# Optimization experiments

Measured on AMD Instinct MI355X. Metric: run time of the kernel, lower is better.

The kernel has to match this reference:

```python
import jax, jax.numpy as jnp
import numpy as np

K = 32
TEMPERATURE = 0.1
RTOL, ATOL = 1e-5, 1e-5


def _embed(x, W1, b1, W2, b2, W3, b3):
    h = jax.nn.gelu(x @ W1.T + b1, approximate=False)
    h = jax.nn.gelu(h @ W2.T + b2, approximate=False)
    return jax.nn.sigmoid(h @ W3.T + b3)


def setup_inputs() -> dict:
    key = jax.random.key(0)
    ks = jax.random.split(key, 9)
    Q, N, D_IN, D_E = 256, 16384, 256, 64
    s = lambda fan_in: 1.0 / np.sqrt(fan_in)
    return {
        "x": jax.random.normal(ks[0], (Q, D_IN), jnp.float32),
        "support_x": jax.random.normal(ks[1], (N, D_IN), jnp.float32),
        "support_labels": jax.random.uniform(ks[2], (N, 1), jnp.float32),
        "W1": jax.random.normal(ks[3], (D_E, D_IN), jnp.float32) * s(D_IN),
        "b1": jax.random.normal(ks[4], (D_E,), jnp.float32) * s(D_IN),
        "W2": jax.random.normal(ks[5], (D_E, D_E), jnp.float32) * s(D_E),
        "b2": jax.random.normal(ks[6], (D_E,), jnp.float32) * s(D_E),
        "W3": jax.random.normal(ks[7], (D_E, D_E), jnp.float32) * s(D_E),
        "b3": jax.random.normal(ks[8], (D_E,), jnp.float32) * s(D_E),
    }


def reference(x, support_x, support_labels, W1, b1, W2, b2, W3, b3):
    # query embeddings [Q, D]; support embeddings [N, D] (set_support is no_grad)
    q = _embed(x, W1, b1, W2, b2, W3, b3)
    s = jax.lax.stop_gradient(_embed(support_x, W1, b1, W2, b2, W3, b3))
    # torch.cdist p=2 via expanded squared distances
    d2 = (jnp.sum(q * q, -1)[:, None] + jnp.sum(s * s, -1)[None, :]
          - 2.0 * (q @ s.T))
    dist = jnp.sqrt(jnp.maximum(d2, 0.0))  # [Q, N]
    # isclose mask: |q - s| <= atol + rtol*|s|, all over feature dim
    close = jnp.abs(q[:, None, :] - s[None, :, :]) <= (ATOL + RTOL * jnp.abs(s)[None, :, :])
    mask = jnp.all(close, axis=-1)  # [Q, N]
    dist = jnp.where(mask, jnp.inf, dist)
    # top-k smallest distances
    neg_top, idx = jax.lax.top_k(-dist, K)  # [Q, K]
    topd = -neg_top
    neighbor_labels = support_labels[idx].squeeze(-1)  # [Q, K]
    weights = jax.nn.softmax(-topd / TEMPERATURE, axis=1)
    return jnp.sum(weights * neighbor_labels, axis=1)  # [Q]
```

## Files before the change

kernel.cpp:

```cpp
#include <hip/hip_runtime.h>
#include <math.h>

#define D_IN   256
#define D_E    64
#define N_SUP  16384
#define NQ     256
#define KSEL   32
#define RTOLC  1e-5f
#define ATOLC  1e-5f
#define INV_T  10.0f

#define CHUNK  1024
#define NCH    16
#define QG     8
#define NQG    32
#define EROWS  16

typedef unsigned long long ull;

__device__ __forceinline__ float gelu_exact(float x) {
    return 0.5f * x * (1.0f + erff(x * 0.70710678118654752440f));
}

__global__ __launch_bounds__(256, 4) void embed_kernel(
    const float* __restrict__ sx, const float* __restrict__ x,
    const float* __restrict__ W1, const float* __restrict__ b1,
    const float* __restrict__ W2, const float* __restrict__ b2,
    const float* __restrict__ W3, const float* __restrict__ b3,
    float* __restrict__ s_emb, float* __restrict__ s_norm,
    float* __restrict__ q_emb, float* __restrict__ q_norm)
{
    __shared__ float xc[2][64][17];
    __shared__ float wc[2][64][68];
    __shared__ float hA[64][17];
    __shared__ float nsq[16][17];

    const int tid = threadIdx.x;
    const int r   = tid & 15;
    const int fg4 = (tid >> 4) * 4;
    const bool isq = blockIdx.x >= (N_SUP / EROWS);
    const float* src = isq ? (x + (size_t)(blockIdx.x - N_SUP / EROWS) * EROWS * D_IN)
                           : (sx + (size_t)blockIdx.x * EROWS * D_IN);

    #define STAGE_X(kc_, b_)                                                   \
        {                                                                      \
            int row_ = tid >> 4, c4_ = tid & 15;                               \
            float4 v_ = *reinterpret_cast<const float4*>(                      \
                src + (size_t)row_ * D_IN + (kc_) * 64 + c4_ * 4);             \
            xc[b_][c4_ * 4 + 0][row_] = v_.x;                                  \
            xc[b_][c4_ * 4 + 1][row_] = v_.y;                                  \
            xc[b_][c4_ * 4 + 2][row_] = v_.z;                                  \
            xc[b_][c4_ * 4 + 3][row_] = v_.w;                                  \
        }
    #define STAGE_W1(kc_, b_)                                                  \
        {                                                                      \
            _Pragma("unroll")                                                  \
            for (int i_ = 0; i_ < 4; ++i_) {                                   \
                int g_ = i_ * 256 + tid;                                       \
                int f_ = g_ >> 4, c4_ = g_ & 15;                               \
                float4 w_ = *reinterpret_cast<const float4*>(                  \
                    W1 + (size_t)f_ * D_IN + (kc_) * 64 + c4_ * 4);            \
                wc[b_][c4_ * 4 + 0][f_] = w_.x;                                \
                wc[b_][c4_ * 4 + 1][f_] = w_.y;                                \
                wc[b_][c4_ * 4 + 2][f_] = w_.z;                                \
                wc[b_][c4_ * 4 + 3][f_] = w_.w;                                \
            }                                                                  \
        }

    STAGE_X(0, 0);
    STAGE_W1(0, 0);
    __syncthreads();

    float4 bv1 = *reinterpret_cast<const float4*>(b1 + fg4);
    float acc[4] = {bv1.x, bv1.y, bv1.z, bv1.w};
    for (int kc = 0; kc < 4; ++kc) {
        const int b = kc & 1;
        if (kc < 3) { STAGE_X(kc + 1, b ^ 1); STAGE_W1(kc + 1, b ^ 1); }
        #pragma unroll 8
        for (int k = 0; k < 64; ++k) {
            float xk = xc[b][k][r];
            float4 wv = *reinterpret_cast<const float4*>(&wc[b][k][fg4]);
            acc[0] = fmaf(wv.x, xk, acc[0]);
            acc[1] = fmaf(wv.y, xk, acc[1]);
            acc[2] = fmaf(wv.z, xk, acc[2]);
            acc[3] = fmaf(wv.w, xk, acc[3]);
        }
        __syncthreads();
    }
    #pragma unroll
    for (int i = 0; i < 4; ++i) hA[fg4 + i][r] = gelu_exact(acc[i]);
    #pragma unroll
    for (int i = 0; i < 4; ++i) {
        int g = i * 256 + tid;
        int f = g >> 4, c4 = g & 15;
        float4 w2 = *reinterpret_cast<const float4*>(W2 + (size_t)f * D_E + c4 * 4);
        wc[0][c4 * 4 + 0][f] = w2.x; wc[0][c4 * 4 + 1][f] = w2.y;
        wc[0][c4 * 4 + 2][f] = w2.z; wc[0][c4 * 4 + 3][f] = w2.w;
        float4 w3 = *reinterpret_cast<const float4*>(W3 + (size_t)f * D_E + c4 * 4);
        wc[1][c4 * 4 + 0][f] = w3.x; wc[1][c4 * 4 + 1][f] = w3.y;
        wc[1][c4 * 4 + 2][f] = w3.z; wc[1][c4 * 4 + 3][f] = w3.w;
    }
    __syncthreads();

    float4 bv2 = *reinterpret_cast<const float4*>(b2 + fg4);
    float a2[4] = {bv2.x, bv2.y, bv2.z, bv2.w};
    #pragma unroll 8
    for (int k = 0; k < D_E; ++k) {
        float hk = hA[k][r];
        float4 wv = *reinterpret_cast<const float4*>(&wc[0][k][fg4]);
        a2[0] = fmaf(wv.x, hk, a2[0]);
        a2[1] = fmaf(wv.y, hk, a2[1]);
        a2[2] = fmaf(wv.z, hk, a2[2]);
        a2[3] = fmaf(wv.w, hk, a2[3]);
    }
    #pragma unroll
    for (int i = 0; i < 4; ++i) xc[0][fg4 + i][r] = gelu_exact(a2[i]);
    __syncthreads();

    float4 bv3 = *reinterpret_cast<const float4*>(b3 + fg4);
    float a3[4] = {bv3.x, bv3.y, bv3.z, bv3.w};
    #pragma unroll 8
    for (int k = 0; k < D_E; ++k) {
        float hk = xc[0][k][r];
        float4 wv = *reinterpret_cast<const float4*>(&wc[1][k][fg4]);
        a3[0] = fmaf(wv.x, hk, a3[0]);
        a3[1] = fmaf(wv.y, hk, a3[1]);
        a3[2] = fmaf(wv.z, hk, a3[2]);
        a3[3] = fmaf(wv.w, hk, a3[3]);
    }
    float e[4];
    float np = 0.0f;
    #pragma unroll
    for (int i = 0; i < 4; ++i) {
        e[i] = 1.0f / (1.0f + expf(-a3[i]));
        np = fmaf(e[i], e[i], np);
    }

    const int rowg = (isq ? (blockIdx.x - N_SUP / EROWS) * EROWS : blockIdx.x * EROWS) + r;
    float* E   = isq ? q_emb  : s_emb;
    float* Nrm = isq ? q_norm : s_norm;
    *reinterpret_cast<float4*>(E + (size_t)rowg * D_E + fg4) =
        make_float4(e[0], e[1], e[2], e[3]);

    nsq[r][fg4 >> 2] = np;
    __syncthreads();
    if (tid < EROWS) {
        float s = nsq[tid][0];
        #pragma unroll
        for (int g = 1; g < 16; ++g) s += nsq[tid][g];
        const int rg = (isq ? (blockIdx.x - N_SUP / EROWS) * EROWS : blockIdx.x * EROWS) + tid;
        Nrm[rg] = s;
    }
    #undef STAGE_X
    #undef STAGE_W1
}

__global__ __launch_bounds__(512, 2) void knn_phaseA(
    const float* __restrict__ s_emb, const float* __restrict__ s_norm,
    const float* __restrict__ q_emb, const float* __restrict__ q_norm,
    const float* __restrict__ labels, ull* __restrict__ cand)
{
    __shared__ float tile[2][64 * 68];
    __shared__ float d2l[QG][1032];
    __shared__ float qs[QG][68];
    __shared__ float qn_l[QG];
    __shared__ ull   win_l[QG][KSEL];

    const int tid  = threadIdx.x;
    const int lane = tid & 63;
    const int wid  = tid >> 6;
    const int qg   = blockIdx.x >> 4;
    const int sc   = blockIdx.x & 15;

    {
        int q = tid >> 6, c = tid & 63;
        qs[q][c] = q_emb[(size_t)(qg * QG + q) * D_E + c];
        if (tid < QG) qn_l[tid] = q_norm[qg * QG + tid];
        #pragma unroll
        for (int i = 0; i < 2; ++i) {
            int g = i * 512 + tid;
            int row = g >> 4, c4 = g & 15;
            float4 v = *reinterpret_cast<const float4*>(
                s_emb + (size_t)(sc * CHUNK + row) * D_E + c4 * 4);
            *reinterpret_cast<float4*>(&tile[0][row * 68 + c4 * 4]) = v;
        }
    }
    __syncthreads();

    const int ql   = lane >> 3;
    const int rsub = lane & 7;
    const int rloc = wid * 8 + rsub;
    const float qn = qn_l[ql];

    for (int s = 0; s < 16; ++s) {
        const int b = s & 1;
        if (s < 15) {
            #pragma unroll
            for (int i = 0; i < 2; ++i) {
                int g = i * 512 + tid;
                int row = g >> 4, c4 = g & 15;
                float4 v = *reinterpret_cast<const float4*>(
                    s_emb + (size_t)(sc * CHUNK + (s + 1) * 64 + row) * D_E + c4 * 4);
                *reinterpret_cast<float4*>(&tile[b ^ 1][row * 68 + c4 * 4]) = v;
            }
        }

        const float* tr = &tile[b][rloc * 68];
        const float* qp = &qs[ql][0];
        float a = 0.0f;
        #pragma unroll
        for (int c = 0; c < 16; ++c) {
            float4 sv = *reinterpret_cast<const float4*>(tr + c * 4);
            float4 qv = *reinterpret_cast<const float4*>(qp + c * 4);
            a = fmaf(qv.x, sv.x, a);
            a = fmaf(qv.y, sv.y, a);
            a = fmaf(qv.z, sv.z, a);
            a = fmaf(qv.w, sv.w, a);
        }
        const int grow = sc * CHUNK + s * 64 + rloc;
        float d2 = fmaxf(qn + s_norm[grow] - 2.0f * a, 0.0f);
        if (d2 < 1e-3f) {
            bool close = true;
            for (int k = 0; k < D_E; ++k) {
                float svk = tr[k];
                close = close && (fabsf(qs[ql][k] - svk) <= (ATOLC + RTOLC * fabsf(svk)));
            }
            if (close) d2 = INFINITY;
        }
        d2l[ql][s * 64 + rloc] = d2;
        __syncthreads();
    }

    ull sk[16];
    #pragma unroll
    for (int j = 0; j < 16; ++j) {
        float d2 = d2l[wid][j * 64 + lane];
        sk[j] = ((ull)__float_as_uint(d2) << 10) | (unsigned)(j * 64 + lane);
    }

    #pragma unroll
    for (int k = 2; k <= 16; k <<= 1) {
        #pragma unroll
        for (int j = k >> 1; j > 0; j >>= 1) {
            #pragma unroll
            for (int i = 0; i < 16; ++i) {
                int ixj = i ^ j;
                if (ixj > i) {
                    if ((i & k) == 0) {
                        ull a_ = sk[i], b_ = sk[ixj];
                        bool c_ = b_ < a_;
                        sk[i] = c_ ? b_ : a_; sk[ixj] = c_ ? a_ : b_;
                    } else {
                        ull a_ = sk[i], b_ = sk[ixj];
                        bool c_ = a_ < b_;
                        sk[i] = c_ ? b_ : a_; sk[ixj] = c_ ? a_ : b_;
                    }
                }
            }
        }
    }

    ull lkey = sk[0];
    unsigned lv = (unsigned)(lkey >> 10);
    for (int it = 0; it < KSEL; ++it) {
        unsigned m = lv;
        #pragma unroll
        for (int off = 1; off < 64; off <<= 1) {
            unsigned o = __shfl_xor(m, off);
            m = o < m ? o : m;
        }
        ull tb = __ballot(lv == m);
        if (__popcll(tb) > 1) {
            unsigned rr = (lv == m) ? (unsigned)(lkey & 1023u) : 0xffffffffu;
            unsigned rm = rr;
            #pragma unroll
            for (int off = 1; off < 64; off <<= 1) {
                unsigned o = __shfl_xor(rm, off);
                rm = o < rm ? o : rm;
            }
            tb = __ballot(rr == rm);
        }
        const int wl = (int)(__ffsll((long long)tb) - 1);
        if (lane == wl) {
            win_l[wid][it] = lkey;
            #pragma unroll
            for (int j = 0; j < 15; ++j) sk[j] = sk[j + 1];
            sk[15] = ~0ull;
            lkey = sk[0];
            lv = (unsigned)(lkey >> 10);
        }
    }

    if (lane < KSEL) {
        ull m = win_l[wid][lane];
        unsigned gidx = (unsigned)(sc * CHUNK) + (unsigned)(m & 1023u);
        float lab = labels[gidx];
        ull* dst = cand + ((size_t)(qg * QG + wid) * NCH + sc) * KSEL;
        dst[lane] = ((ull)(unsigned)(m >> 10) << 32) | (ull)__float_as_uint(lab);
    }
}

__global__ __launch_bounds__(256) void knn_phaseB(
    const ull* __restrict__ cand, float* __restrict__ out)
{
    const int lane = threadIdx.x & 63;
    const int wid  = threadIdx.x >> 6;
    const int q    = blockIdx.x * 4 + wid;

    const bool act = lane < NCH;
    const ull* lst = cand + ((size_t)q * NCH + (lane & 15)) * KSEL;
    int ptr = 0;
    ull cur = act ? lst[0] : ~0ull;

    float d0 = 0.0f, sw = 0.0f, sl = 0.0f;
    for (int it = 0; it < KSEL; ++it) {
        unsigned mv = (unsigned)(cur >> 32);
        unsigned ml = (unsigned)cur;
        #pragma unroll
        for (int off = 1; off < 16; off <<= 1) {
            unsigned ov = __shfl_xor(mv, off);
            unsigned ol = __shfl_xor(ml, off);
            bool take = (ov < mv) || (ov == mv && (lane & off));
            mv = take ? ov : mv;
            ml = take ? ol : ml;
        }
        ull b = __ballot(act && (unsigned)(cur >> 32) == mv);
        int wl = (int)(__ffsll((long long)b) - 1);
        if (lane == wl) {
            ++ptr;
            cur = (ptr < KSEL) ? lst[ptr] : ~0ull;
        }
        if (lane == 0) {
            float d = sqrtf(__uint_as_float(mv));
            if (it == 0) d0 = d;
            float w = expf((d0 - d) * INV_T);
            sw += w;
            sl += w * __uint_as_float(ml);
        }
    }
    if (lane == 0) out[q] = sl / sw;
}

extern "C" void kernel_launch(void* const* d_in, const int* in_sizes, int n_in,
                              void* d_out, int out_size, void* d_ws, size_t ws_size,
                              hipStream_t stream) {
    const float* x      = (const float*)d_in[0];
    const float* sx     = (const float*)d_in[1];
    const float* labels = (const float*)d_in[2];
    const float* W1     = (const float*)d_in[3];
    const float* b1     = (const float*)d_in[4];
    const float* W2     = (const float*)d_in[5];
    const float* b2     = (const float*)d_in[6];
    const float* W3     = (const float*)d_in[7];
    const float* b3     = (const float*)d_in[8];
    float* out = (float*)d_out;

    float* ws     = (float*)d_ws;
    float* s_emb  = ws;
    float* s_norm = s_emb + N_SUP * D_E;
    float* q_emb  = s_norm + N_SUP;
    float* q_norm = q_emb + NQ * D_E;
    ull*   cand   = (ull*)(q_norm + NQ);

    embed_kernel<<<(N_SUP + NQ) / EROWS, 256, 0, stream>>>(
        sx, x, W1, b1, W2, b2, W3, b3, s_emb, s_norm, q_emb, q_norm);
    knn_phaseA<<<NQG * NCH, 512, 0, stream>>>(s_emb, s_norm, q_emb, q_norm,
                                              labels, cand);
    knn_phaseB<<<NQ / 4, 256, 0, stream>>>(cand, out);
}
```

Before: 111.5 us.

## Register-tile embedding MLP 4x4 and process two queries per wave in kNN

The embedding kernel now has each block handle 64 rows, and each thread computes a 4x4 register tile. This raises arithmetic intensity and cuts the shared-memory loads per FMA. The kNN phase A now gives each wavefront two queries. Distances stay in registers instead of a shared d2 buffer, query vectors are read from global through a uniform pointer, and the next tile is prefetched into registers. The larger blocks and higher register use lower occupancy (launch bounds 2 and 1), and halving the block count for phase A reduces parallelism.

```diff
diff --git a/kernel.cpp b/kernel.cpp
--- a/kernel.cpp
+++ b/kernel.cpp
@@ -12,9 +12,8 @@
 
 #define CHUNK  1024
 #define NCH    16
-#define QG     8
-#define NQG    32
-#define EROWS  16
+#define QG     16
+#define NQG    16
 
 typedef unsigned long long ull;
 
@@ -22,7 +21,7 @@
     return 0.5f * x * (1.0f + erff(x * 0.70710678118654752440f));
 }
 
-__global__ __launch_bounds__(256, 4) void embed_kernel(
+__global__ __launch_bounds__(256, 2) void embed_kernel(
     const float* __restrict__ sx, const float* __restrict__ x,
     const float* __restrict__ W1, const float* __restrict__ b1,
     const float* __restrict__ W2, const float* __restrict__ b2,
@@ -30,27 +29,31 @@
     float* __restrict__ s_emb, float* __restrict__ s_norm,
     float* __restrict__ q_emb, float* __restrict__ q_norm)
 {
-    __shared__ float xc[2][64][17];
+    __shared__ float xc[2][64][68];
     __shared__ float wc[2][64][68];
-    __shared__ float hA[64][17];
-    __shared__ float nsq[16][17];
+    __shared__ float nsq[64][17];
 
     const int tid = threadIdx.x;
-    const int r   = tid & 15;
-    const int fg4 = (tid >> 4) * 4;
-    const bool isq = blockIdx.x >= (N_SUP / EROWS);
-    const float* src = isq ? (x + (size_t)(blockIdx.x - N_SUP / EROWS) * EROWS * D_IN)
-                           : (sx + (size_t)blockIdx.x * EROWS * D_IN);
+    const int rg  = tid >> 4;
+    const int fg  = tid & 15;
+    const bool isq = blockIdx.x >= (N_SUP / 64);
+    const int rowbase = isq ? (int)(blockIdx.x - N_SUP / 64) * 64
+                            : (int)blockIdx.x * 64;
+    const float* src = (isq ? x : sx) + (size_t)rowbase * D_IN;
 
     #define STAGE_X(kc_, b_)                                                   \
         {                                                                      \
-            int row_ = tid >> 4, c4_ = tid & 15;                               \
-            float4 v_ = *reinterpret_cast<const float4*>(                      \
-                src + (size_t)row_ * D_IN + (kc_) * 64 + c4_ * 4);             \
-            xc[b_][c4_ * 4 + 0][row_] = v_.x;                                  \
-            xc[b_][c4_ * 4 + 1][row_] = v_.y;                                  \
-            xc[b_][c4_ * 4 + 2][row_] = v_.z;                                  \
-            xc[b_][c4_ * 4 + 3][row_] = v_.w;                                  \
+            _Pragma("unroll")                                                  \
+            for (int i_ = 0; i_ < 4; ++i_) {                                   \
+                int g_ = i_ * 256 + tid;                                       \
+                int row_ = g_ >> 4, c4_ = g_ & 15;                             \
+                float4 v_ = *reinterpret_cast<const float4*>(                  \
+                    src + (size_t)row_ * D_IN + (kc_) * 64 + c4_ * 4);         \
+                xc[b_][c4_ * 4 + 0][row_] = v_.x;                              \
+                xc[b_][c4_ * 4 + 1][row_] = v_.y;                              \
+                xc[b_][c4_ * 4 + 2][row_] = v_.z;                              \
+                xc[b_][c4_ * 4 + 3][row_] = v_.w;                              \
+            }                                                                  \
         }
     #define STAGE_W1(kc_, b_)                                                  \
         {                                                                      \
@@ -66,104 +69,127 @@
                 wc[b_][c4_ * 4 + 3][f_] = w_.w;                                \
             }                                                                  \
         }
-
-    STAGE_X(0, 0);
-    STAGE_W1(0, 0);
-    __syncthreads();
-
-    float4 bv1 = *reinterpret_cast<const float4*>(b1 + fg4);
-    float acc[4] = {bv1.x, bv1.y, bv1.z, bv1.w};
+    #define STAGE_WSQ(Wp_, b_)                                                 \
+        {                                                                      \
+            _Pragma("unroll")                                                  \
+            for (int i_ = 0; i_ < 4; ++i_) {                                   \
+                int g_ = i_ * 256 + tid;                                       \
+                int f_ = g_ >> 4, c4_ = g_ & 15;                               \
+                float4 w_ = *reinterpret_cast<const float4*>(                  \
+                    (Wp_) + (size_t)f_ * D_E + c4_ * 4);                       \
+                wc[b_][c4_ * 4 + 0][f_] = w_.x;                                \
+                wc[b_][c4_ * 4 + 1][f_] = w_.y;                                \
+                wc[b_][c4_ * 4 + 2][f_] = w_.z;                                \
+                wc[b_][c4_ * 4 + 3][f_] = w_.w;                                \
+            }                                                                  \
+        }
+    #define GEMM64(XB_, WB_, ACC_)                                             \
+        {                                                                      \
+            _Pragma("unroll 8")                                                \
+            for (int k_ = 0; k_ < 64; ++k_) {                                  \
+                float4 xv_ = *reinterpret_cast<const float4*>(&XB_[k_][rg * 4]); \
+                float4 wv_ = *reinterpret_cast<const float4*>(&WB_[k_][fg * 4]); \
+                ACC_[0][0] = fmaf(wv_.x, xv_.x, ACC_[0][0]);                   \
+                ACC_[0][1] = fmaf(wv_.y, xv_.x, ACC_[0][1]);                   \
+                ACC_[0][2] = fmaf(wv_.z, xv_.x, ACC_[0][2]);                   \
+                ACC_[0][3] = fmaf(wv_.w, xv_.x, ACC_[0][3]);                   \
+                ACC_[1][0] = fmaf(wv_.x, xv_.y, ACC_[1][0]);                   \
+                ACC_[1][1] = fmaf(wv_.y, xv_.y, ACC_[1][1]);                   \
+                ACC_[1][2] = fmaf(wv_.z, xv_.y, ACC_[1][2]);                   \
+                ACC_[1][3] = fmaf(wv_.w, xv_.y, ACC_[1][3]);                   \
+                ACC_[2][0] = fmaf(wv_.x, xv_.z, ACC_[2][0]);                   \
+                ACC_[2][1] = fmaf(wv_.y, xv_.z, ACC_[2][1]);                   \
+                ACC_[2][2] = fmaf(wv_.z, xv_.z, ACC_[2][2]);                   \
+                ACC_[2][3] = fmaf(wv_.w, xv_.z, ACC_[2][3]);                   \
+                ACC_[3][0] = fmaf(wv_.x, xv_.w, ACC_[3][0]);                   \
+                ACC_[3][1] = fmaf(wv_.y, xv_.w, ACC_[3][1]);                   \
+                ACC_[3][2] = fmaf(wv_.z, xv_.w, ACC_[3][2]);                   \
+                ACC_[3][3] = fmaf(wv_.w, xv_.w, ACC_[3][3]);                   \
+            }                                                                  \
+        }
+
+    float4 bv1 = *reinterpret_cast<const float4*>(b1 + fg * 4);
+    float acc[4][4];
+    #pragma unroll
+    for (int j = 0; j < 4; ++j) {
+        acc[j][0] = bv1.x; acc[j][1] = bv1.y; acc[j][2] = bv1.z; acc[j][3] = bv1.w;
+    }
+    STAGE_X(0, 0); STAGE_W1(0, 0);
+    __syncthreads();
+    #pragma unroll
     for (int kc = 0; kc < 4; ++kc) {
         const int b = kc & 1;
         if (kc < 3) { STAGE_X(kc + 1, b ^ 1); STAGE_W1(kc + 1, b ^ 1); }
-        #pragma unroll 8
-        for (int k = 0; k < 64; ++k) {
-            float xk = xc[b][k][r];
-            float4 wv = *reinterpret_cast<const float4*>(&wc[b][k][fg4]);
-            acc[0] = fmaf(wv.x, xk, acc[0]);
-            acc[1] = fmaf(wv.y, xk, acc[1]);
-            acc[2] = fmaf(wv.z, xk, acc[2]);
-            acc[3] = fmaf(wv.w, xk, acc[3]);
-        }
+        GEMM64(xc[b], wc[b], acc);
         __syncthreads();
     }
-    #pragma unroll
-    for (int i = 0; i < 4; ++i) hA[fg4 + i][r] = gelu_exact(acc[i]);
-    #pragma unroll
-    for (int i = 0; i < 4; ++i) {
-        int g = i * 256 + tid;
-        int f = g >> 4, c4 = g & 15;
-        float4 w2 = *reinterpret_cast<const float4*>(W2 + (size_t)f * D_E + c4 * 4);
-        wc[0][c4 * 4 + 0][f] = w2.x; wc[0][c4 * 4 + 1][f] = w2.y;
-        wc[0][c4 * 4 + 2][f] = w2.z; wc[0][c4 * 4 + 3][f] = w2.w;
-        float4 w3 = *reinterpret_cast<const float4*>(W3 + (size_t)f * D_E + c4 * 4);
-        wc[1][c4 * 4 + 0][f] = w3.x; wc[1][c4 * 4 + 1][f] = w3.y;
-        wc[1][c4 * 4 + 2][f] = w3.z; wc[1][c4 * 4 + 3][f] = w3.w;
-    }
-    __syncthreads();
-
-    float4 bv2 = *reinterpret_cast<const float4*>(b2 + fg4);
-    float a2[4] = {bv2.x, bv2.y, bv2.z, bv2.w};
-    #pragma unroll 8
-    for (int k = 0; k < D_E; ++k) {
-        float hk = hA[k][r];
-        float4 wv = *reinterpret_cast<const float4*>(&wc[0][k][fg4]);
-        a2[0] = fmaf(wv.x, hk, a2[0]);
-        a2[1] = fmaf(wv.y, hk, a2[1]);
-        a2[2] = fmaf(wv.z, hk, a2[2]);
-        a2[3] = fmaf(wv.w, hk, a2[3]);
-    }
-    #pragma unroll
-    for (int i = 0; i < 4; ++i) xc[0][fg4 + i][r] = gelu_exact(a2[i]);
-    __syncthreads();
-
-    float4 bv3 = *reinterpret_cast<const float4*>(b3 + fg4);
-    float a3[4] = {bv3.x, bv3.y, bv3.z, bv3.w};
-    #pragma unroll 8
-    for (int k = 0; k < D_E; ++k) {
-        float hk = xc[0][k][r];
-        float4 wv = *reinterpret_cast<const float4*>(&wc[1][k][fg4]);
-        a3[0] = fmaf(wv.x, hk, a3[0]);
-        a3[1] = fmaf(wv.y, hk, a3[1]);
-        a3[2] = fmaf(wv.z, hk, a3[2]);
-        a3[3] = fmaf(wv.w, hk, a3[3]);
-    }
-    float e[4];
-    float np = 0.0f;
-    #pragma unroll
-    for (int i = 0; i < 4; ++i) {
-        e[i] = 1.0f / (1.0f + expf(-a3[i]));
-        np = fmaf(e[i], e[i], np);
-    }
-
-    const int rowg = (isq ? (blockIdx.x - N_SUP / EROWS) * EROWS : blockIdx.x * EROWS) + r;
+
+    #pragma unroll
+    for (int j = 0; j < 4; ++j)
+        #pragma unroll
+        for (int i = 0; i < 4; ++i)
+            xc[0][fg * 4 + i][rg * 4 + j] = gelu_exact(acc[j][i]);
+    STAGE_WSQ(W2, 0);
+    STAGE_WSQ(W3, 1);
+    __syncthreads();
+
+    float4 bv2 = *reinterpret_cast<const float4*>(b2 + fg * 4);
+    float a2[4][4];
+    #pragma unroll
+    for (int j = 0; j < 4; ++j) {
+        a2[j][0] = bv2.x; a2[j][1] = bv2.y; a2[j][2] = bv2.z; a2[j][3] = bv2.w;
+    }
+    GEMM64(xc[0], wc[0], a2);
+    __syncthreads();
+    #pragma unroll
+    for (int j = 0; j < 4; ++j)
+        #pragma unroll
+        for (int i = 0; i < 4; ++i)
+            xc[1][fg * 4 + i][rg * 4 + j] = gelu_exact(a2[j][i]);
+    __syncthreads();
+
+    float4 bv3 = *reinterpret_cast<const float4*>(b3 + fg * 4);
+    float a3[4][4];
+    #pragma unroll
+    for (int j = 0; j < 4; ++j) {
+        a3[j][0] = bv3.x; a3[j][1] = bv3.y; a3[j][2] = bv3.z; a3[j][3] = bv3.w;
+    }
+    GEMM64(xc[1], wc[1], a3);
+
     float* E   = isq ? q_emb  : s_emb;
     float* Nrm = isq ? q_norm : s_norm;
-    *reinterpret_cast<float4*>(E + (size_t)rowg * D_E + fg4) =
-        make_float4(e[0], e[1], e[2], e[3]);
-
-    nsq[r][fg4 >> 2] = np;
-    __syncthreads();
-    if (tid < EROWS) {
-        float s = nsq[tid][0];
-        #pragma unroll
-        for (int g = 1; g < 16; ++g) s += nsq[tid][g];
-        const int rg = (isq ? (blockIdx.x - N_SUP / EROWS) * EROWS : blockIdx.x * EROWS) + tid;
-        Nrm[rg] = s;
+    #pragma unroll
+    for (int j = 0; j < 4; ++j) {
+        float e0 = 1.0f / (1.0f + expf(-a3[j][0]));
+        float e1 = 1.0f / (1.0f + expf(-a3[j][1]));
+        float e2 = 1.0f / (1.0f + expf(-a3[j][2]));
+        float e3 = 1.0f / (1.0f + expf(-a3[j][3]));
+        *reinterpret_cast<float4*>(E + (size_t)(rowbase + rg * 4 + j) * D_E + fg * 4)
+            = make_float4(e0, e1, e2, e3);
+        a3[j][0] = fmaf(e0, e0, fmaf(e1, e1, fmaf(e2, e2, e3 * e3)));
+    }
+    __syncthreads();
+    #pragma unroll
+    for (int j = 0; j < 4; ++j) nsq[rg * 4 + j][fg] = a3[j][0];
+    __syncthreads();
+    if (tid < 64) {
+        float s = 0.0f;
+        #pragma unroll
+        for (int g = 0; g < 16; ++g) s += nsq[tid][g];
+        Nrm[rowbase + tid] = s;
     }
     #undef STAGE_X
     #undef STAGE_W1
+    #undef STAGE_WSQ
+    #undef GEMM64
 }
 
-__global__ __launch_bounds__(512, 2) void knn_phaseA(
+__global__ __launch_bounds__(512, 1) void knn_phaseA(
     const float* __restrict__ s_emb, const float* __restrict__ s_norm,
     const float* __restrict__ q_emb, const float* __restrict__ q_norm,
     const float* __restrict__ labels, ull* __restrict__ cand)
 {
     __shared__ float tile[2][64 * 68];
-    __shared__ float d2l[QG][1032];
-    __shared__ float qs[QG][68];
-    __shared__ float qn_l[QG];
     __shared__ ull   win_l[QG][KSEL];
 
     const int tid  = threadIdx.x;
@@ -171,132 +197,139 @@
     const int wid  = tid >> 6;
     const int qg   = blockIdx.x >> 4;
     const int sc   = blockIdx.x & 15;
-
-    {
-        int q = tid >> 6, c = tid & 63;
-        qs[q][c] = q_emb[(size_t)(qg * QG + q) * D_E + c];
-        if (tid < QG) qn_l[tid] = q_norm[qg * QG + tid];
-        #pragma unroll
-        for (int i = 0; i < 2; ++i) {
-            int g = i * 512 + tid;
-            int row = g >> 4, c4 = g & 15;
-            float4 v = *reinterpret_cast<const float4*>(
-                s_emb + (size_t)(sc * CHUNK + row) * D_E + c4 * 4);
-            *reinterpret_cast<float4*>(&tile[0][row * 68 + c4 * 4]) = v;
-        }
-    }
-    __syncthreads();
-
-    const int ql   = lane >> 3;
-    const int rsub = lane & 7;
-    const int rloc = wid * 8 + rsub;
-    const float qn = qn_l[ql];
-
+    const int qiu  = __builtin_amdgcn_readfirstlane(qg * QG + 2 * wid);
+    const float* q0 = q_emb + (size_t)qiu * D_E;
+    const float* q1 = q0 + D_E;
+    const float  qn0 = q_norm[qiu];
+    const float  qn1 = q_norm[qiu + 1];
+
+    #pragma unroll
+    for (int i = 0; i < 2; ++i) {
+        int g = i * 512 + tid;
+        int row = g >> 4, c4 = g & 15;
+        float4 v = *reinterpret_cast<const float4*>(
+            s_emb + (size_t)(sc * CHUNK + row) * D_E + c4 * 4);
+        *reinterpret_cast<float4*>(&tile[0][row * 68 + c4 * 4]) = v;
+    }
+    __syncthreads();
+
+    float d2a[16], d2b[16];
+    #pragma unroll
     for (int s = 0; s < 16; ++s) {
         const int b = s & 1;
+        float4 p0, p1;
         if (s < 15) {
-            #pragma unroll
-            for (int i = 0; i < 2; ++i) {
-                int g = i * 512 + tid;
-                int row = g >> 4, c4 = g & 15;
-                float4 v = *reinterpret_cast<const float4*>(
-                    s_emb + (size_t)(sc * CHUNK + (s + 1) * 64 + row) * D_E + c4 * 4);
-                *reinterpret_cast<float4*>(&tile[b ^ 1][row * 68 + c4 * 4]) = v;
-            }
-        }
-
-        const float* tr = &tile[b][rloc * 68];
-        const float* qp = &qs[ql][0];
-        float a = 0.0f;
+            p0 = *reinterpret_cast<const float4*>(
+                s_emb + (size_t)(sc * CHUNK + (s + 1) * 64 + (tid >> 4)) * D_E + (tid & 15) * 4);
+            p1 = *reinterpret_cast<const float4*>(
+                s_emb + (size_t)(sc * CHUNK + (s + 1) * 64 + ((512 + tid) >> 4)) * D_E + (tid & 15) * 4);
+        }
+        const float* tr = &tile[b][lane * 68];
+        float a0 = 0.0f, a1 = 0.0f;
         #pragma unroll
         for (int c = 0; c < 16; ++c) {
             float4 sv = *reinterpret_cast<const float4*>(tr + c * 4);
-            float4 qv = *reinterpret_cast<const float4*>(qp + c * 4);
-            a = fmaf(qv.x, sv.x, a);
-            a = fmaf(qv.y, sv.y, a);
-            a = fmaf(qv.z, sv.z, a);
-            a = fmaf(qv.w, sv.w, a);
-        }
-        const int grow = sc * CHUNK + s * 64 + rloc;
-        float d2 = fmaxf(qn + s_norm[grow] - 2.0f * a, 0.0f);
-        if (d2 < 1e-3f) {
+            a0 = fmaf(q0[c * 4 + 0], sv.x, a0);
+            a0 = fmaf(q0[c * 4 + 1], sv.y, a0);
+            a0 = fmaf(q0[c * 4 + 2], sv.z, a0);
+            a0 = fmaf(q0[c * 4 + 3], sv.w, a0);
+            a1 = fmaf(q1[c * 4 + 0], sv.x, a1);
+            a1 = fmaf(q1[c * 4 + 1], sv.y, a1);
+            a1 = fmaf(q1[c * 4 + 2], sv.z, a1);
+            a1 = fmaf(q1[c * 4 + 3], sv.w, a1);
+        }
+        const int grow = sc * CHUNK + s * 64 + lane;
+        const float sn = s_norm[grow];
+        float d20 = fmaxf(qn0 + sn - 2.0f * a0, 0.0f);
+        float d21 = fmaxf(qn1 + sn - 2.0f * a1, 0.0f);
+        if (d20 < 1e-3f) {
             bool close = true;
             for (int k = 0; k < D_E; ++k) {
                 float svk = tr[k];
-                close = close && (fabsf(qs[ql][k] - svk) <= (ATOLC + RTOLC * fabsf(svk)));
-            }
-            if (close) d2 = INFINITY;
-        }
-        d2l[ql][s * 64 + rloc] = d2;
+                close = close && (fabsf(q0[k] - svk) <= (ATOLC + RTOLC * fabsf(svk)));
+            }
+            if (close) d20 = INFINITY;
+        }
+        if (d21 < 1e-3f) {
+            bool close = true;
+            for (int k = 0; k < D_E; ++k) {
+                float svk = tr[k];
+                close = close && (fabsf(q1[k] - svk) <= (ATOLC + RTOLC * fabsf(svk)));
+            }
+            if (close) d21 = INFINITY;
+        }
+        d2a[s] = d20;
+        d2b[s] = d21;
+        if (s < 15) {
+            *reinterpret_cast<float4*>(&tile[b ^ 1][(tid >> 4) * 68 + (tid & 15) * 4]) = p0;
+            *reinterpret_cast<float4*>(&tile[b ^ 1][((512 + tid) >> 4) * 68 + (tid & 15) * 4]) = p1;
+        }
         __syncthreads();
     }
 
-    ull sk[16];
-    #pragma unroll
-    for (int j = 0; j < 16; ++j) {
-        float d2 = d2l[wid][j * 64 + lane];
-        sk[j] = ((ull)__float_as_uint(d2) << 10) | (unsigned)(j * 64 + lane);
-    }
-
-    #pragma unroll
-    for (int k = 2; k <= 16; k <<= 1) {
-        #pragma unroll
-        for (int j = k >> 1; j > 0; j >>= 1) {
+    #pragma unroll
+    for (int h = 0; h < 2; ++h) {
+        ull sk[16];
+        #pragma unroll
+        for (int j = 0; j < 16; ++j) {
+            float d2 = h ? d2b[j] : d2a[j];
+            sk[j] = ((ull)__float_as_uint(d2) << 10) | (unsigned)(j * 64 + lane);
+        }
+        #pragma unroll
+        for (int k = 2; k <= 16; k <<= 1) {
             #pragma unroll
-            for (int i = 0; i < 16; ++i) {
-                int ixj = i ^ j;
-                if (ixj > i) {
-                    if ((i & k) == 0) {
+            for (int j = k >> 1; j > 0; j >>= 1) {
+                #pragma unroll
+                for (int i = 0; i < 16; ++i) {
+                    int ixj = i ^ j;
+                    if (ixj > i) {
                         ull a_ = sk[i], b_ = sk[ixj];
-                        bool c_ = b_ < a_;
-                        sk[i] = c_ ? b_ : a_; sk[ixj] = c_ ? a_ : b_;
-                    } else {
-                        ull a_ = sk[i], b_ = sk[ixj];
-                        bool c_ = a_ < b_;
+                        bool up = (i & k) == 0;
+                        bool c_ = up ? (b_ < a_) : (a_ < b_);
                         sk[i] = c_ ? b_ : a_; sk[ixj] = c_ ? a_ : b_;
                     }
                 }
             }
         }
-    }
-
-    ull lkey = sk[0];
-    unsigned lv = (unsigned)(lkey >> 10);
-    for (int it = 0; it < KSEL; ++it) {
-        unsigned m = lv;
-        #pragma unroll
-        for (int off = 1; off < 64; off <<= 1) {
-            unsigned o = __shfl_xor(m, off);
-            m = o < m ? o : m;
-        }
-        ull tb = __ballot(lv == m);
-        if (__popcll(tb) > 1) {
-            unsigned rr = (lv == m) ? (unsigned)(lkey & 1023u) : 0xffffffffu;
-            unsigned rm = rr;
+        ull lkey = sk[0];
+        for (int it = 0; it < KSEL; ++it) {
+            unsigned lv = (unsigned)(lkey >> 10);
+            unsigned m = lv;
             #pragma unroll
             for (int off = 1; off < 64; off <<= 1) {
-                unsigned o = __shfl_xor(rm, off);
-                rm = o < rm ? o : rm;
-            }
-            tb = __ballot(rr == rm);
-        }
-        const int wl = (int)(__ffsll((long long)tb) - 1);
-        if (lane == wl) {
-            win_l[wid][it] = lkey;
-            #pragma unroll
-            for (int j = 0; j < 15; ++j) sk[j] = sk[j + 1];
-            sk[15] = ~0ull;
-            lkey = sk[0];
-            lv = (unsigned)(lkey >> 10);
-        }
-    }
-
-    if (lane < KSEL) {
-        ull m = win_l[wid][lane];
+                unsigned o = __shfl_xor(m, off);
+                m = o < m ? o : m;
+            }
+            ull tb = __ballot(lv == m);
+            if (__popcll(tb) > 1) {
+                unsigned rr = (lv == m) ? (unsigned)(lkey & 1023u) : 0xffffffffu;
+                unsigned rm = rr;
+                #pragma unroll
+                for (int off = 1; off < 64; off <<= 1) {
+                    unsigned o = __shfl_xor(rm, off);
+                    rm = o < rm ? o : rm;
+                }
+                tb = __ballot(rr == rm);
+            }
+            const int wl = (int)(__ffsll((long long)tb) - 1);
+            if (lane == wl) {
+                win_l[2 * wid + h][it] = lkey;
+                #pragma unroll
+                for (int j = 0; j < 15; ++j) sk[j] = sk[j + 1];
+                sk[15] = ~0ull;
+                lkey = sk[0];
+            }
+        }
+    }
+
+    {
+        const int h = lane >> 5;
+        const int e = lane & 31;
+        ull m = win_l[2 * wid + h][e];
         unsigned gidx = (unsigned)(sc * CHUNK) + (unsigned)(m & 1023u);
         float lab = labels[gidx];
-        ull* dst = cand + ((size_t)(qg * QG + wid) * NCH + sc) * KSEL;
-        dst[lane] = ((ull)(unsigned)(m >> 10) << 32) | (ull)__float_as_uint(lab);
+        ull* dst = cand + ((size_t)(qiu + h) * NCH + sc) * KSEL;
+        dst[e] = ((ull)(unsigned)(m >> 10) << 32) | (ull)__float_as_uint(lab);
     }
 }
 
@@ -357,12 +390,12 @@
 
     float* ws     = (float*)d_ws;
     float* s_emb  = ws;
-    float* s_norm = s_emb + N_SUP * D_E;
+    float* s_norm = s_emb + (size_t)N_SUP * D_E;
     float* q_emb  = s_norm + N_SUP;
-    float* q_norm = q_emb + NQ * D_E;
+    float* q_norm = q_emb + (size_t)NQ * D_E;
     ull*   cand   = (ull*)(q_norm + NQ);
 
-    embed_kernel<<<(N_SUP + NQ) / EROWS, 256, 0, stream>>>(
+    embed_kernel<<<(N_SUP + NQ) / 64, 256, 0, stream>>>(
         sx, x, W1, b1, W2, b2, W3, b3, s_emb, s_norm, q_emb, q_norm);
     knn_phaseA<<<NQG * NCH, 512, 0, stream>>>(s_emb, s_norm, q_emb, q_norm,
                                               labels, cand);
```

After: 101.3 us. -9.2%, faster.
